# Kernel tuning notes

Measured on AMD Instinct MI355X. Metric: run time of the kernel, lower is better.

Reference implementation:

```python
import jax, jax.numpy as jnp
import numpy as np

N_CIR, N_DIS, D, H = 585, 88, 128, 8
E_CC, E_DD = 20000, 3000
EPS = 1e-16


def _gcn(x, src, dst, ew, W, b, N):
    # PyG GCNConv: add self-loops (weight 1), symmetric normalization, x @ W, scatter-add, + bias
    loop = jnp.arange(N)
    s = jnp.concatenate([src, loop])
    d = jnp.concatenate([dst, loop])
    w = jnp.concatenate([ew, jnp.ones((N,), ew.dtype)])
    deg = jax.ops.segment_sum(w, d, num_segments=N)
    dinv = jnp.where(deg > 0, jax.lax.rsqrt(deg), 0.0)
    norm = dinv[s] * w * dinv[d]                      # [E+N]
    h = x @ W                                         # [N,D]
    out = jax.ops.segment_sum(h[s] * norm[:, None], d, num_segments=N)
    return out + b


def _gat(x, src, dst, ea, W, a_src, a_dst, a_edge, We, b, N):
    # PyG GATConv(heads=H, concat=False, edge_dim=1): self-loops with mean edge_attr fill,
    # leaky_relu attention logits, segment softmax over destination, mean over heads, + bias
    loop = jnp.arange(N)
    s = jnp.concatenate([src, loop])
    d = jnp.concatenate([dst, loop])
    ea = jnp.concatenate([ea, jnp.broadcast_to(ea.mean(0, keepdims=True), (N, ea.shape[1]))], 0)
    h = (x @ W).reshape(N, H, D)                      # [N,H,D]
    e = (ea @ We).reshape(-1, H, D)                   # [E+N,H,D]
    alpha = (h * a_src).sum(-1)[s] + (h * a_dst).sum(-1)[d] + (e * a_edge).sum(-1)
    alpha = jax.nn.leaky_relu(alpha, 0.2)             # [E+N,H]
    amax = jax.ops.segment_max(alpha, d, num_segments=N)
    ex = jnp.exp(alpha - amax[d])
    den = jax.ops.segment_sum(ex, d, num_segments=N)
    alpha = ex / (den[d] + EPS)
    out = jax.ops.segment_sum(h[s] * alpha[:, :, None], d, num_segments=N)  # [N,H,D]
    return out.mean(1) + b


def _branch(x, edges, mat, gw1, gb1, aw, asrc, adst, aedge, awe, ab, gw2, gb2, N):
    src, dst = edges[0], edges[1]
    ew = mat[src, dst]                                # gather edge weights from dense matrix
    f1 = jax.nn.relu(_gcn(x, src, dst, ew, gw1, gb1, N))
    att = jax.nn.relu(_gat(f1, src, dst, ew[:, None], aw, asrc, adst, aedge, awe, ab, N))
    f2 = jax.nn.relu(_gcn(att, src, dst, ew, gw2, gb2, N))
    return f1, f2


def _cnn(f1, f2, Wk, b):
    # Conv2d(2,256,(128,1)) over [1,2,128,N] == per-node GEMM over (2,128) then view/transpose
    Xv = jnp.stack([f1.T, f2.T])                      # [2,D,N]
    return jnp.einsum('ock,ckn->no', Wk[..., 0], Xv) + b  # [N,256]


def setup_inputs():
    ks = jax.random.split(jax.random.key(0), 24)
    rn = lambda i, sh, s=1.0: jax.random.normal(ks[i], sh, jnp.float32) * s
    w = 0.08  # ~glorot scale for fan-in 128
    return {
        'x_cir': rn(0, (N_CIR, D)),
        'x_dis': rn(1, (N_DIS, D)),
        'cc_matrix': jax.random.uniform(ks[2], (N_CIR, N_CIR), jnp.float32),
        'dd_matrix': jax.random.uniform(ks[3], (N_DIS, N_DIS), jnp.float32),
        'gcn_c1_w': rn(4, (D, D), w), 'gcn_c1_b': jnp.zeros((D,), jnp.float32),
        'gat_c_w': rn(5, (D, H * D), w), 'gat_c_asrc': rn(6, (H, D), w),
        'gat_c_adst': rn(7, (H, D), w), 'gat_c_aedge': rn(8, (H, D), w),
        'gat_c_we': rn(9, (1, H * D), w), 'gat_c_b': jnp.zeros((D,), jnp.float32),
        'gcn_c2_w': rn(10, (D, D), w), 'gcn_c2_b': jnp.zeros((D,), jnp.float32),
        'gcn_d1_w': rn(11, (D, D), w), 'gcn_d1_b': jnp.zeros((D,), jnp.float32),
        'gat_d_w': rn(12, (D, H * D), w), 'gat_d_asrc': rn(13, (H, D), w),
        'gat_d_adst': rn(14, (H, D), w), 'gat_d_aedge': rn(15, (H, D), w),
        'gat_d_we': rn(16, (1, H * D), w), 'gat_d_b': jnp.zeros((D,), jnp.float32),
        'gcn_d2_w': rn(17, (D, D), w), 'gcn_d2_b': jnp.zeros((D,), jnp.float32),
        'conv_c_w': rn(18, (256, 2, D, 1), w), 'conv_c_b': jnp.zeros((256,), jnp.float32),
        'conv_d_w': rn(19, (256, 2, D, 1), w), 'conv_d_b': jnp.zeros((256,), jnp.float32),
        'cc_edges': jax.random.randint(ks[20], (2, E_CC), 0, N_CIR),
        'dd_edges': jax.random.randint(ks[21], (2, E_DD), 0, N_DIS),
    }


def reference(x_cir, x_dis, cc_matrix, dd_matrix,
              gcn_c1_w, gcn_c1_b, gat_c_w, gat_c_asrc, gat_c_adst, gat_c_aedge, gat_c_we, gat_c_b,
              gcn_c2_w, gcn_c2_b,
              gcn_d1_w, gcn_d1_b, gat_d_w, gat_d_asrc, gat_d_adst, gat_d_aedge, gat_d_we, gat_d_b,
              gcn_d2_w, gcn_d2_b,
              conv_c_w, conv_c_b, conv_d_w, conv_d_b,
              cc_edges, dd_edges):
    c1, c2 = _branch(x_cir, cc_edges, cc_matrix, gcn_c1_w, gcn_c1_b, gat_c_w, gat_c_asrc,
                     gat_c_adst, gat_c_aedge, gat_c_we, gat_c_b, gcn_c2_w, gcn_c2_b, N_CIR)
    d1, d2 = _branch(x_dis, dd_edges, dd_matrix, gcn_d1_w, gcn_d1_b, gat_d_w, gat_d_asrc,
                     gat_d_adst, gat_d_aedge, gat_d_we, gat_d_b, gcn_d2_w, gcn_d2_b, N_DIS)
    cir_fea = _cnn(c1, c2, conv_c_w, conv_c_b)        # [585,256]
    dis_fea = _cnn(d1, d2, conv_d_w, conv_d_b)        # [88,256]
    return cir_fea @ dis_fea.T, cir_fea, dis_fea
```

## Files before the change

kernel.cpp:

```cpp
#include <hip/hip_runtime.h>

constexpr int NCIR = 585;
constexpr int NDIS = 88;
constexpr int NT   = NCIR + NDIS;
constexpr int DIM  = 128;
constexpr int NH   = 8;
constexpr int ECC  = 20000;
constexpr int EDD  = 3000;
constexpr int ET   = ECC + EDD;
constexpr int CO   = 256;
constexpr int CAP  = 256;
constexpr int F1C  = (NCIR + 3) / 4;
constexpr int F1D  = (NDIS + 3) / 4;
constexpr int NG   = F1C + F1D;
constexpr int GBK  = (ET + 255) / 256;
constexpr int GEMB4 = (NT + 3) / 4;

__device__ __forceinline__ int decode_cnt(unsigned raw){
  return (int)(raw >= 0xA0000000u ? raw - 0xAAAAAAAAu : raw);
}

struct P {
  const float *x_c, *x_d, *mat_c, *mat_d;
  const float *g1w_c, *g1b_c, *aw_c, *as_c, *ad_c, *ae_c, *we_c, *ab_c, *g2w_c, *g2b_c;
  const float *g1w_d, *g1b_d, *aw_d, *as_d, *ad_d, *ae_d, *we_d, *ab_d, *g2w_d, *g2b_d;
  const float *cw_c, *cb_c, *cw_d, *cb_d;
  const int *csrc, *cdst, *dsrc, *ddst;
  float *hs, *hd, *h, *f1, *hg, *fill_w, *psc, *psd, *wdeg, *wdall;
  unsigned *cnt, *done;
  int *fill_s;
  float *out_score, *out_cir, *out_dis;
};

__global__ __launch_bounds__(256) void k_gg(P p){
  __shared__ float sbuf[512];
  int b = blockIdx.x, t = threadIdx.x;
  if (b < GBK){
    float* r0 = sbuf;
    float* r1 = sbuf + 256;
    int e = b * 256 + t;
    float wc = 0.0f, wdv = 0.0f;
    if (e < ET){
      float w; int s, d;
      if (e < ECC){
        s = p.csrc[e]; d = p.cdst[e];
        w = p.mat_c[s * NCIR + d]; wc = w;
      } else {
        int el = e - ECC;
        s = NCIR + p.dsrc[el]; d = NCIR + p.ddst[el];
        w = p.mat_d[(s - NCIR) * NDIS + (d - NCIR)]; wdv = w;
      }
      int pos = decode_cnt(atomicAdd(&p.cnt[d], 1u));
      if (pos < CAP){
        p.fill_s[d * CAP + pos] = s;
        p.fill_w[d * CAP + pos] = w;
      }
      atomicAdd(&p.wdeg[d], w);
    }
    r0[t] = wc; r1[t] = wdv;
    __syncthreads();
    for (int st = 128; st; st >>= 1){
      if (t < st){ r0[t] += r0[t + st]; r1[t] += r1[t + st]; }
      __syncthreads();
    }
    if (t == 0){ p.psc[b] = r0[0]; p.psd[b] = r1[0]; }
  } else if (b < GBK + GEMB4){
    int base = (b - GBK) * 4;
    for (int idx = t; idx < 512; idx += 256){
      int n = idx >> 7, k2 = idx & 127;
      int u = base + n;
      float v = 0.0f;
      if (u < NT) v = (u >= NCIR) ? p.x_d[(u - NCIR) * DIM + k2]
                                  : p.x_c[u * DIM + k2];
      sbuf[idx] = v;
    }
    __syncthreads();
    int k = t & 127, np = t >> 7;
    int u0 = base + 2 * np, u1 = u0 + 1;
    bool mixed = (base < NCIR) && (base + 3 >= NCIR);
    if (!mixed){
      const float* W = (base >= NCIR) ? p.g1w_d : p.g1w_c;
      float a0 = 0.0f, a1 = 0.0f;
      #pragma unroll 8
      for (int c = 0; c < DIM; ++c){
        float wv = W[c * DIM + k];
        a0 += sbuf[2 * np * DIM + c] * wv;
        a1 += sbuf[(2 * np + 1) * DIM + c] * wv;
      }
      if (u0 < NT) p.h[(size_t)u0 * DIM + k] = a0;
      if (u1 < NT) p.h[(size_t)u1 * DIM + k] = a1;
    } else {
      for (int r = 0; r < 2; ++r){
        int u = base + 2 * np + r;
        const float* W = (u >= NCIR) ? p.g1w_d : p.g1w_c;
        float a = 0.0f;
        #pragma unroll 8
        for (int c = 0; c < DIM; ++c) a += sbuf[(2 * np + r) * DIM + c] * W[c * DIM + k];
        p.h[(size_t)u * DIM + k] = a;
      }
    }
  } else {
    int brn = b - (GBK + GEMB4);
    const float* We = brn ? p.we_d : p.we_c;
    const float* Ae = brn ? p.ae_d : p.ae_c;
    int hh = t >> 5, l = t & 31;
    float v = 0.0f;
    #pragma unroll
    for (int q = l; q < DIM; q += 32) v += We[hh * DIM + q] * Ae[hh * DIM + q];
    #pragma unroll
    for (int off = 16; off; off >>= 1) v += __shfl_down(v, off, 32);
    if (l == 0) p.wdall[brn * NH + hh] = v;
  }
}

__global__ __launch_bounds__(256) void k_aggproj(P p){
  __shared__ int   deg4[4];
  __shared__ float dv4[4];
  __shared__ int   s4[4][CAP];
  __shared__ float nrm4[4][CAP];
  __shared__ __align__(16) float apart[8][DIM];
  __shared__ float a_sh[4][DIM];
  __shared__ float wred[4][8];
  int b = blockIdx.x, t = threadIdx.x;
  int ng = b >> 2, ct = b & 3;
  int base, count, br;
  if (ng < F1C){ base = ng * 4; count = min(4, NCIR - base); br = 0; }
  else { base = NCIR + (ng - F1C) * 4; count = 4; br = 1; }
  if (t < 4){
    if (t < count){
      int u = base + t;
      deg4[t] = min(decode_cnt(p.cnt[u]), CAP);
      dv4[t]  = rsqrtf(1.0f + p.wdeg[u]);
    } else deg4[t] = 0;
  }
  __syncthreads();
  for (int idx = t; idx < 4 * CAP; idx += 256){
    int nn = idx >> 8, j = idx & (CAP - 1);
    if (j < deg4[nn]){
      int u = base + nn;
      int s = p.fill_s[u * CAP + j];
      s4[nn][j] = s;
      nrm4[nn][j] = rsqrtf(1.0f + p.wdeg[s]) * p.fill_w[u * CAP + j] * dv4[nn];
    }
  }
  __syncthreads();
  {
    int slot = t >> 5, lane = t & 31;
    int nn = slot >> 1, jp = slot & 1;
    float4 acc4 = {0.f, 0.f, 0.f, 0.f};
    if (nn < count){
      if (jp == 0){
        int u = base + nn;
        float sc = dv4[nn] * dv4[nn];
        const float4* B14 = (const float4*)(br ? p.g1b_d : p.g1b_c);
        const float4* h4  = (const float4*)(p.h + (size_t)u * DIM);
        float4 bb = B14[lane], hv = h4[lane];
        acc4.x = bb.x + hv.x * sc; acc4.y = bb.y + hv.y * sc;
        acc4.z = bb.z + hv.z * sc; acc4.w = bb.w + hv.w * sc;
      }
      int deg = deg4[nn];
      #pragma unroll 4
      for (int j = jp; j < deg; j += 2){
        const float4* hr = (const float4*)(p.h + (size_t)s4[nn][j] * DIM);
        float w = nrm4[nn][j];
        float4 hv = hr[lane];
        acc4.x += hv.x * w; acc4.y += hv.y * w;
        acc4.z += hv.z * w; acc4.w += hv.w * w;
      }
    }
    ((float4*)apart[slot])[lane] = acc4;
  }
  __syncthreads();
  {
    int n2 = t >> 7, k = t & 127;
    for (int r = 0; r < 2; ++r){
      int nn = n2 + r * 2;
      float sum = apart[nn * 2][k] + apart[nn * 2 + 1][k];
      if (nn < count && ct == 0) p.f1[(size_t)(base + nn) * DIM + k] = sum;
      a_sh[nn][k] = (nn < count) ? fmaxf(sum, 0.0f) : 0.0f;
    }
  }
  __syncthreads();
  const float* W = (br ? p.aw_d : p.aw_c) + ct * 256 + t;
  float acc[4] = {0.f, 0.f, 0.f, 0.f};
  #pragma unroll 4
  for (int c = 0; c < DIM; ++c){
    float w = W[c * 1024];
    acc[0] += a_sh[0][c] * w; acc[1] += a_sh[1][c] * w;
    acc[2] += a_sh[2][c] * w; acc[3] += a_sh[3][c] * w;
  }
  int col = ct * 256 + t;
  for (int n = 0; n < count; ++n)
    p.hg[(size_t)(base + n) * 1024 + col] = acc[n];
  const float* As = br ? p.as_d : p.as_c;
  const float* Ad = br ? p.ad_d : p.ad_c;
  float av = As[col], dw = Ad[col];
  int w = t >> 6;
  #pragma unroll
  for (int n = 0; n < 4; ++n){
    float sdot = acc[n] * av, ddot = acc[n] * dw;
    #pragma unroll
    for (int off = 32; off; off >>= 1){
      sdot += __shfl_down(sdot, off, 64);
      ddot += __shfl_down(ddot, off, 64);
    }
    if ((t & 63) == 0){ wred[w][n * 2] = sdot; wred[w][n * 2 + 1] = ddot; }
  }
  __syncthreads();
  if (t < 16){
    int g = t >> 3, v = t & 7, n = v >> 1, isd = v & 1;
    if (n < count){
      float sum = wred[g * 2][v] + wred[g * 2 + 1][v];
      float* dst = isd ? p.hd : p.hs;
      dst[(base + n) * NH + ct * 2 + g] = sum;
    }
  }
}

__global__ __launch_bounds__(256) void k_att(P p){
  __shared__ float den_sh[NH], hd_sh[NH], inv_sh[NH], wself_sh[NH], wd_sh[NH];
  __shared__ float slw_sh;
  __shared__ int   s_all[CAP];
  __shared__ float w_all[CAP];
  __shared__ float alpha_all[CAP * NH];
  __shared__ __align__(16) float hacc[NH][DIM];
  __shared__ float attv[DIM];
  __shared__ float part[2][DIM];
  int d = blockIdx.x, t = threadIdx.x;
  int g = t >> 7, k = t & 127;
  int br = d >= NCIR;
  int wv = t >> 6, lane64 = t & 63;
  if (t < NH){
    den_sh[t] = 0.0f;
    hd_sh[t]  = p.hd[d * NH + t];
    wd_sh[t]  = p.wdall[br * NH + t];
  }
  if (wv == 0){
    const float* ps = br ? p.psd : p.psc;
    float v = (lane64 < GBK ? ps[lane64] : 0.0f) + (lane64 + 64 < GBK ? ps[lane64 + 64] : 0.0f);
    #pragma unroll
    for (int off = 32; off; off >>= 1) v += __shfl_down(v, off, 64);
    if (lane64 == 0) slw_sh = v / (br ? (float)EDD : (float)ECC);
  }
  int deg = min(decode_cnt(p.cnt[d]), CAP);
  for (int j = t; j < deg; j += 256){
    s_all[j] = p.fill_s[d * CAP + j];
    w_all[j] = p.fill_w[d * CAP + j];
  }
  __syncthreads();
  int bound = deg * NH;
  for (int i0 = 0; i0 < bound; i0 += 256){
    int idx = i0 + t;
    float ex = 0.0f;
    if (idx < bound){
      int j = idx >> 3, hh = idx & 7;
      float a = p.hs[s_all[j] * NH + hh] + hd_sh[hh] + w_all[j] * wd_sh[hh];
      a = a > 0.0f ? a : 0.2f * a;
      ex = expf(a);
      alpha_all[idx] = ex;
    }
    float v = ex;
    v += __shfl_xor(v, 8, 64);
    v += __shfl_xor(v, 16, 64);
    v += __shfl_xor(v, 32, 64);
    if (lane64 < 8) atomicAdd(&den_sh[lane64], v);
  }
  __syncthreads();
  if (t < NH){
    float a = p.hs[d * NH + t] + hd_sh[t] + slw_sh * wd_sh[t];
    a = a > 0.0f ? a : 0.2f * a;
    float ex = expf(a);
    float inv = 1.0f / (den_sh[t] + ex + 1e-16f) * 0.125f;
    inv_sh[t] = inv;
    wself_sh[t] = ex * inv;
  }
  __syncthreads();
  {
    int hh = t >> 5, lane = t & 31;
    float sc = inv_sh[hh];
    const float4* rd = (const float4*)(p.hg + (size_t)d * 1024 + hh * DIM);
    float ws = wself_sh[hh];
    float4 v = rd[lane];
    float4 acc4 = {ws * v.x, ws * v.y, ws * v.z, ws * v.w};
    #pragma unroll 4
    for (int jj = 0; jj < deg; ++jj){
      const float4* r = (const float4*)(p.hg + (size_t)s_all[jj] * 1024 + hh * DIM);
      float a = alpha_all[jj * NH + hh] * sc;
      float4 hv = r[lane];
      acc4.x += a * hv.x; acc4.y += a * hv.y;
      acc4.z += a * hv.z; acc4.w += a * hv.w;
    }
    ((float4*)hacc[hh])[lane] = acc4;
  }
  __syncthreads();
  if (g == 0){
    float s0 = 0.0f;
    #pragma unroll
    for (int hh = 0; hh < NH; ++hh) s0 += hacc[hh][k];
    attv[k] = fmaxf((br ? p.ab_d : p.ab_c)[k] + s0, 0.0f);
  }
  __syncthreads();
  const float* W = br ? p.g2w_d : p.g2w_c;
  float h2 = 0.0f;
  #pragma unroll 8
  for (int c = g * 64; c < g * 64 + 64; ++c) h2 += attv[c] * W[c * DIM + k];
  part[g][k] = h2;
  __syncthreads();
  if (g == 0) p.h[d * DIM + k] = part[0][k] + part[1][k];
}

__global__ __launch_bounds__(256) void k_fuse2f(P p){
  __shared__ int   s_all[CAP];
  __shared__ float nrm_all[CAP];
  __shared__ __align__(16) float red[8][DIM];
  __shared__ __align__(16) float s12[2 * DIM];
  int b = blockIdx.x, t = threadIdx.x;
  int br = b < NDIS;
  int u  = br ? NCIR + b : b - NDIS;
  float* out = br ? p.out_dis + (size_t)b * CO
                  : p.out_cir + (size_t)(b - NDIS) * CO;
  int deg = min(decode_cnt(p.cnt[u]), CAP);
  float dvu = rsqrtf(1.0f + p.wdeg[u]);
  for (int j = t; j < deg; j += 256){
    int s = p.fill_s[u * CAP + j];
    s_all[j] = s;
    nrm_all[j] = rsqrtf(1.0f + p.wdeg[s]) * p.fill_w[u * CAP + j] * dvu;
  }
  __syncthreads();
  {
    int slot = t >> 5, lane = t & 31;
    float4 acc4 = {0.f, 0.f, 0.f, 0.f};
    if (slot == 0){
      const float4* B24 = (const float4*)(br ? p.g2b_d : p.g2b_c);
      const float4* h4  = (const float4*)(p.h + (size_t)u * DIM);
      float sc = dvu * dvu;
      float4 bb = B24[lane], hv = h4[lane];
      acc4.x = bb.x + hv.x * sc; acc4.y = bb.y + hv.y * sc;
      acc4.z = bb.z + hv.z * sc; acc4.w = bb.w + hv.w * sc;
    }
    #pragma unroll 4
    for (int j = slot; j < deg; j += 8){
      const float4* hr = (const float4*)(p.h + (size_t)s_all[j] * DIM);
      float w = nrm_all[j];
      float4 hv = hr[lane];
      acc4.x += hv.x * w; acc4.y += hv.y * w;
      acc4.z += hv.z * w; acc4.w += hv.w * w;
    }
    ((float4*)red[slot])[lane] = acc4;
  }
  __syncthreads();
  if (t < DIM){
    float sum = red[0][t] + red[1][t] + red[2][t] + red[3][t]
              + red[4][t] + red[5][t] + red[6][t] + red[7][t];
    s12[DIM + t] = fmaxf(sum, 0.0f);
    s12[t]       = fmaxf(p.f1[(size_t)u * DIM + t], 0.0f);
  }
  __syncthreads();
  const float4* W4 = (const float4*)((br ? p.cw_d : p.cw_c) + (size_t)t * 2 * DIM);
  const float4* sv = (const float4*)s12;
  float acc = (br ? p.cb_d : p.cb_c)[t];
  #pragma unroll 8
  for (int q = 0; q < 64; ++q){
    float4 w = W4[q], s = sv[q];
    acc += w.x * s.x + w.y * s.y + w.z * s.z + w.w * s.w;
  }
  out[t] = acc;
  if (br){
    __syncthreads();
    if (t == 0){
      __threadfence();
      atomicAdd(p.done, 1u);
    }
    return;
  }
  float* ci  = &red[0][0];
  float* fin = ci + CO;
  ci[t] = acc;
  if (t == 0){
    while (decode_cnt(__hip_atomic_load(p.done, __ATOMIC_ACQUIRE,
                                        __HIP_MEMORY_SCOPE_AGENT)) < NDIS){
      __builtin_amdgcn_s_sleep(16);
    }
  }
  __syncthreads();
  int half = t >> 7, j = t & 127;
  if (j < NDIS){
    const float4* dr = (const float4*)(p.out_dis + (size_t)j * CO + half * DIM);
    const float4* cc = (const float4*)(ci + half * DIM);
    float a2 = 0.0f;
    #pragma unroll 8
    for (int q = 0; q < 32; ++q){
      float4 a = cc[q], bb = dr[q];
      a2 += a.x * bb.x + a.y * bb.y + a.z * bb.z + a.w * bb.w;
    }
    fin[half * NDIS + j] = a2;
  }
  __syncthreads();
  if (t < NDIS)
    p.out_score[(size_t)(b - NDIS) * NDIS + t] = fin[t] + fin[NDIS + t];
}

extern "C" void kernel_launch(void* const* d_in, const int* in_sizes, int n_in,
                              void* d_out, int out_size, void* d_ws, size_t ws_size,
                              hipStream_t stream){
  P p;
  typedef const float* F;
  p.x_c   = (F)d_in[0];  p.x_d   = (F)d_in[1];
  p.mat_c = (F)d_in[2];  p.mat_d = (F)d_in[3];
  p.g1w_c = (F)d_in[4];  p.g1b_c = (F)d_in[5];
  p.aw_c  = (F)d_in[6];  p.as_c  = (F)d_in[7];  p.ad_c = (F)d_in[8];
  p.ae_c  = (F)d_in[9];  p.we_c  = (F)d_in[10]; p.ab_c = (F)d_in[11];
  p.g2w_c = (F)d_in[12]; p.g2b_c = (F)d_in[13];
  p.g1w_d = (F)d_in[14]; p.g1b_d = (F)d_in[15];
  p.aw_d  = (F)d_in[16]; p.as_d  = (F)d_in[17]; p.ad_d = (F)d_in[18];
  p.ae_d  = (F)d_in[19]; p.we_d  = (F)d_in[20]; p.ab_d = (F)d_in[21];
  p.g2w_d = (F)d_in[22]; p.g2b_d = (F)d_in[23];
  p.cw_c  = (F)d_in[24]; p.cb_c  = (F)d_in[25];
  p.cw_d  = (F)d_in[26]; p.cb_d  = (F)d_in[27];
  const int* cc_edges = (const int*)d_in[28];
  const int* dd_edges = (const int*)d_in[29];
  p.csrc = cc_edges;  p.cdst = cc_edges + ECC;
  p.dsrc = dd_edges;  p.ddst = dd_edges + EDD;

  float* out = (float*)d_out;
  p.out_score = out;
  p.out_cir   = out + NCIR * NDIS;
  p.out_dis   = p.out_cir + NCIR * CO;

  float* w = (float*)d_ws;
  auto alloc = [&](size_t n){ float* q = w; w += n; return q; };
  p.wdeg   = alloc(676);
  p.cnt    = (unsigned*)alloc(676);
  p.done   = (unsigned*)alloc(4);
  p.psc    = alloc(92);
  p.psd    = alloc(92);
  p.wdall  = alloc(16);
  p.hs     = alloc((size_t)NT * NH);
  p.hd     = alloc((size_t)NT * NH);
  p.h      = alloc((size_t)NT * DIM);
  p.f1     = alloc((size_t)NT * DIM);
  p.hg     = alloc((size_t)NT * 1024);
  p.fill_w = alloc((size_t)NT * CAP);
  p.fill_s = (int*)alloc((size_t)NT * CAP);

  k_gg     <<<GBK + GEMB4 + 2, 256, 0, stream>>>(p);
  k_aggproj<<<NG * 4,          256, 0, stream>>>(p);
  k_att    <<<NT,              256, 0, stream>>>(p);
  k_fuse2f <<<NT,              256, 0, stream>>>(p);
}
```

Baseline: 215.2 us.

## Split fused score computation into separate final kernel instead of spin-wait

```diff
diff --git a/kernel.cpp b/kernel.cpp
--- a/kernel.cpp
+++ b/kernel.cpp
@@ -27,7 +27,7 @@
   const float *cw_c, *cb_c, *cw_d, *cb_d;
   const int *csrc, *cdst, *dsrc, *ddst;
   float *hs, *hd, *h, *f1, *hg, *fill_w, *psc, *psd, *wdeg, *wdall;
-  unsigned *cnt, *done;
+  unsigned *cnt;
   int *fill_s;
   float *out_score, *out_cir, *out_dis;
 };
@@ -309,16 +309,15 @@
   if (g == 0) p.h[d * DIM + k] = part[0][k] + part[1][k];
 }
 
-__global__ __launch_bounds__(256) void k_fuse2f(P p){
+__global__ __launch_bounds__(256) void k_fuse2(P p){
   __shared__ int   s_all[CAP];
   __shared__ float nrm_all[CAP];
   __shared__ __align__(16) float red[8][DIM];
   __shared__ __align__(16) float s12[2 * DIM];
-  int b = blockIdx.x, t = threadIdx.x;
-  int br = b < NDIS;
-  int u  = br ? NCIR + b : b - NDIS;
-  float* out = br ? p.out_dis + (size_t)b * CO
-                  : p.out_cir + (size_t)(b - NDIS) * CO;
+  int u = blockIdx.x, t = threadIdx.x;
+  int br = u >= NCIR;
+  float* out = br ? p.out_dis + (size_t)(u - NCIR) * CO
+                  : p.out_cir + (size_t)u * CO;
   int deg = min(decode_cnt(p.cnt[u]), CAP);
   float dvu = rsqrtf(1.0f + p.wdeg[u]);
   for (int j = t; j < deg; j += 256){
@@ -365,39 +364,28 @@
     acc += w.x * s.x + w.y * s.y + w.z * s.z + w.w * s.w;
   }
   out[t] = acc;
-  if (br){
-    __syncthreads();
-    if (t == 0){
-      __threadfence();
-      atomicAdd(p.done, 1u);
-    }
-    return;
-  }
-  float* ci  = &red[0][0];
-  float* fin = ci + CO;
-  ci[t] = acc;
-  if (t == 0){
-    while (decode_cnt(__hip_atomic_load(p.done, __ATOMIC_ACQUIRE,
-                                        __HIP_MEMORY_SCOPE_AGENT)) < NDIS){
-      __builtin_amdgcn_s_sleep(16);
-    }
-  }
+}
+
+__global__ void k_final(P p){
+  __shared__ __align__(16) float ci[CO];
+  __shared__ float fin[2][NDIS];
+  int i = blockIdx.x, t = threadIdx.x;
+  ci[t] = p.out_cir[(size_t)i * CO + t];
   __syncthreads();
   int half = t >> 7, j = t & 127;
   if (j < NDIS){
     const float4* dr = (const float4*)(p.out_dis + (size_t)j * CO + half * DIM);
     const float4* cc = (const float4*)(ci + half * DIM);
-    float a2 = 0.0f;
+    float acc = 0.0f;
     #pragma unroll 8
     for (int q = 0; q < 32; ++q){
-      float4 a = cc[q], bb = dr[q];
-      a2 += a.x * bb.x + a.y * bb.y + a.z * bb.z + a.w * bb.w;
-    }
-    fin[half * NDIS + j] = a2;
-  }
-  __syncthreads();
-  if (t < NDIS)
-    p.out_score[(size_t)(b - NDIS) * NDIS + t] = fin[t] + fin[NDIS + t];
+      float4 a = cc[q], b = dr[q];
+      acc += a.x * b.x + a.y * b.y + a.z * b.z + a.w * b.w;
+    }
+    fin[half][j] = acc;
+  }
+  __syncthreads();
+  if (t < NDIS) p.out_score[(size_t)i * NDIS + t] = fin[0][t] + fin[1][t];
 }
 
 extern "C" void kernel_launch(void* const* d_in, const int* in_sizes, int n_in,
@@ -431,7 +419,6 @@
   auto alloc = [&](size_t n){ float* q = w; w += n; return q; };
   p.wdeg   = alloc(676);
   p.cnt    = (unsigned*)alloc(676);
-  p.done   = (unsigned*)alloc(4);
   p.psc    = alloc(92);
   p.psd    = alloc(92);
   p.wdall  = alloc(16);
@@ -446,5 +433,6 @@
   k_gg     <<<GBK + GEMB4 + 2, 256, 0, stream>>>(p);
   k_aggproj<<<NG * 4,          256, 0, stream>>>(p);
   k_att    <<<NT,              256, 0, stream>>>(p);
-  k_fuse2f <<<NT,              256, 0, stream>>>(p);
-}
+  k_fuse2  <<<NT,              256, 0, stream>>>(p);
+  k_final  <<<NCIR,            256, 0, stream>>>(p);
+}
```

After: 194.7 us. -9.5%, faster.
